# Kernel tuning notes

Measured on AMD Instinct MI355X. Metric: run time of the kernel, lower is better.

The kernel has to match this reference:

```python
import jax, jax.numpy as jnp
import numpy as np
import math

NUM_HEADS = 16
EMBED = 1024
B, S = 128, 512


def setup_inputs() -> dict:
    key = jax.random.key(0)
    ks = jax.random.split(key, 9)
    scale = 1.0 / math.sqrt(EMBED)
    return {
        "queries": jax.random.normal(ks[0], (B, S, EMBED), dtype=jnp.float32),
        "keys": jax.random.normal(ks[1], (B, S, EMBED), dtype=jnp.float32),
        "values": jax.random.normal(ks[2], (B, S, EMBED), dtype=jnp.float32),
        "Wq": jax.random.normal(ks[3], (EMBED, EMBED), dtype=jnp.float32) * scale,
        "bq": jax.random.normal(ks[4], (EMBED,), dtype=jnp.float32) * scale,
        "Wk": jax.random.normal(ks[5], (EMBED, EMBED), dtype=jnp.float32) * scale,
        "bk": jax.random.normal(ks[6], (EMBED,), dtype=jnp.float32) * scale,
        "Wv": jax.random.normal(ks[7], (EMBED, EMBED), dtype=jnp.float32) * scale,
        "bv": jax.random.normal(ks[8], (EMBED,), dtype=jnp.float32) * scale,
    }


def reference(queries, keys, values, Wq, bq, Wk, bk, Wv, bv):
    H = NUM_HEADS
    E = queries.shape[-1]
    d = E // H
    # torch nn.Linear: y = x @ W.T + b
    q = queries @ Wq.T + bq  # [B, S, E]
    k = keys @ Wk.T + bk
    v = values @ Wv.T + bv
    n_q = q.shape[1]
    n_k = k.shape[1]
    n_v = v.shape[1]
    # Faithful to the original: reshape with seq-len as the LEADING dim,
    # which reinterprets the (B, S, E) buffer as (S, B, H, d).
    q = q.reshape(n_q, -1, H, d)  # [S, B, H, d]
    k = k.reshape(n_k, -1, H, d)
    # attention over the second (batch-like) axis; scores: [S, H, B, B]
    scores = jnp.einsum('nqhd,nkhd->nhqk', q, k) / math.sqrt(d)
    attn = jax.nn.softmax(scores, axis=-1)
    v = v.reshape(n_v, -1, H, d)  # [S, B, H, d]
    out = jnp.einsum('nhql,nlhd->nqhd', attn, v)  # [S, B, H, d]
    n_a = out.shape[0]
    return out.reshape(-1, n_a, H * d)  # [B, S, E]
```

## Files before the change

### kernel.cpp

```cpp
#include <hip/hip_runtime.h>
#include <hip/hip_bf16.h>

typedef unsigned short u16;
typedef __attribute__((ext_vector_type(8))) short bf16x8;
typedef __attribute__((ext_vector_type(4))) float f32x4;
typedef __attribute__((ext_vector_type(4))) float vfloat4;
typedef __attribute__((ext_vector_type(4))) unsigned short ushort4v;
typedef __attribute__((ext_vector_type(8))) unsigned short ushort8v;

#define DEV __device__ __forceinline__
#define AS1 __attribute__((address_space(1)))
#define AS3 __attribute__((address_space(3)))

#define BARRIER()  __builtin_amdgcn_s_barrier()
#define LGKM0()    asm volatile("s_waitcnt lgkmcnt(0)" ::: "memory")
#define VMCNT2()   asm volatile("s_waitcnt vmcnt(2)" ::: "memory")
#define SCHED0()   __builtin_amdgcn_sched_barrier(0)

DEV u16 f2bf(float f) {
    union { float f; unsigned u; } v; v.f = f;
    unsigned r = v.u + 0x7FFFu + ((v.u >> 16) & 1u);
    return (u16)(r >> 16);
}

DEV void gload_lds16(const void* g, void* l) {
    __builtin_amdgcn_global_load_lds((const AS1 unsigned int*)g,
                                     (AS3 unsigned int*)l, 16, 0, 0);
}

static constexpr int KDIM = 1024;
static constexpr int NROW = 65536;

__global__ __launch_bounds__(256)
void cvt_f32_bf16(const float* __restrict__ src, u16* __restrict__ dst, unsigned n8)
{
    unsigned stride = gridDim.x * blockDim.x;
    for (unsigned i = blockIdx.x * blockDim.x + threadIdx.x; i < n8; i += stride) {
        size_t base = (size_t)i * 8;
        vfloat4 a = *(const vfloat4*)(src + base);
        vfloat4 b = *(const vfloat4*)(src + base + 4);
        ushort8v o;
#pragma unroll
        for (int j = 0; j < 4; ++j) { o[j] = f2bf(a[j]); o[j + 4] = f2bf(b[j]); }
        *(ushort8v*)(dst + base) = o;
    }
}

__global__ __launch_bounds__(512)
__attribute__((amdgpu_waves_per_eu(1, 2)))
void proj_gemm_8ph(const u16* __restrict__ X, const u16* __restrict__ W,
                   const float* __restrict__ bias, u16* __restrict__ Y)
{
    __shared__ __align__(16) u16 As[2][256 * 64];
    __shared__ __align__(16) u16 Bs[2][256 * 64];

    int bx = blockIdx.x;
    int wg = (bx & 7) * 128 + (bx >> 3);
    int bm = wg >> 2;
    int bn = wg & 3;

    int tid  = threadIdx.x;
    int lane = tid & 63;
    int wid  = tid >> 6;
    int wm   = wid >> 2;
    int wn   = wid & 3;
    int l15  = lane & 15;
    int l4   = lane >> 4;

    const u16* Xp = X + (size_t)bm * 256 * KDIM;
    const u16* Wp = W + (size_t)bn * 256 * KDIM;

    int srow_in = tid >> 3;
    int scol16  = (tid & 7) ^ (srow_in & 7);

    f32x4 acc[8][4] = {};

#define STAGE(lds, gbase, slot, h, kt)                                           \
    {                                                                            \
        const u16* src_ = (gbase) + (size_t)((h) * 128 + srow_in) * KDIM         \
                          + (kt) * 64 + scol16 * 8;                              \
        gload_lds16(src_, &lds[slot][((h) * 128 + wid * 8) * 64]);               \
        gload_lds16(src_ + (size_t)64 * KDIM,                                    \
                    &lds[slot][((h) * 128 + 64 + wid * 8) * 64]);                \
    }

#define READ_AF(slot, mh)                                                        \
    {                                                                            \
        _Pragma("unroll")                                                        \
        for (int mi = 0; mi < 4; ++mi) {                                         \
            int row = wm * 128 + (mh) * 64 + mi * 16 + l15;                      \
            unsigned o0 = (unsigned)(row * 128 + l4 * 16) ^ (unsigned)((row & 7) << 4); \
            af[mi][0] = *(const bf16x8*)((const char*)As[slot] + o0);            \
            af[mi][1] = *(const bf16x8*)((const char*)As[slot] + (o0 ^ 64u));    \
        }                                                                        \
    }

#define READ_BF(dst, slot, nh)                                                   \
    {                                                                            \
        _Pragma("unroll")                                                        \
        for (int ni = 0; ni < 2; ++ni) {                                         \
            int row = wn * 64 + (nh) * 32 + ni * 16 + l15;                       \
            unsigned o0 = (unsigned)(row * 128 + l4 * 16) ^ (unsigned)((row & 7) << 4); \
            dst[ni][0] = *(const bf16x8*)((const char*)Bs[slot] + o0);           \
            dst[ni][1] = *(const bf16x8*)((const char*)Bs[slot] + (o0 ^ 64u));   \
        }                                                                        \
    }

#define MFMA_Q(mlo, bb, nlo)                                                     \
    __builtin_amdgcn_s_setprio(1);                                               \
    _Pragma("unroll")                                                            \
    for (int mi = 0; mi < 4; ++mi) {                                             \
        _Pragma("unroll")                                                        \
        for (int ni = 0; ni < 2; ++ni) {                                         \
            _Pragma("unroll")                                                    \
            for (int kk = 0; kk < 2; ++kk)                                       \
                acc[(mlo) + mi][(nlo) + ni] = __builtin_amdgcn_mfma_f32_16x16x32_bf16( \
                    af[mi][kk], bb[ni][kk], acc[(mlo) + mi][(nlo) + ni], 0, 0, 0); \
        }                                                                        \
    }                                                                            \
    __builtin_amdgcn_s_setprio(0);

    STAGE(As, Xp, 0, 0, 0);
    STAGE(As, Xp, 0, 1, 0);
    STAGE(Bs, Wp, 0, 0, 0);
    STAGE(Bs, Wp, 0, 1, 0);
    STAGE(As, Xp, 1, 0, 1);
    VMCNT2();
    BARRIER();

    for (int it = 0; it < 8; ++it) {
        int kt1 = 2 * it + 1;
        int kt2 = (2 * it + 2 < 16) ? 2 * it + 2 : 15;
        int kt3 = (2 * it + 3 < 16) ? 2 * it + 3 : 15;
        bf16x8 af[4][2], b0[2][2], b1[2][2];

        READ_AF(0, 0); READ_BF(b0, 0, 0);
        STAGE(As, Xp, 1, 1, kt1);
        BARRIER(); LGKM0(); SCHED0();
        MFMA_Q(0, b0, 0);
        BARRIER();

        READ_BF(b1, 0, 1);
        STAGE(Bs, Wp, 1, 0, kt1);
        BARRIER(); LGKM0(); SCHED0();
        MFMA_Q(0, b1, 2);
        BARRIER();

        READ_AF(0, 1);
        STAGE(Bs, Wp, 1, 1, kt1);
        BARRIER(); LGKM0(); SCHED0();
        MFMA_Q(4, b1, 2);
        BARRIER();

        STAGE(As, Xp, 0, 0, kt2);
        MFMA_Q(4, b0, 0);
        VMCNT2();
        BARRIER();

        READ_AF(1, 0); READ_BF(b0, 1, 0);
        STAGE(As, Xp, 0, 1, kt2);
        BARRIER(); LGKM0(); SCHED0();
        MFMA_Q(0, b0, 0);
        BARRIER();

        READ_BF(b1, 1, 1);
        STAGE(Bs, Wp, 0, 0, kt2);
        BARRIER(); LGKM0(); SCHED0();
        MFMA_Q(0, b1, 2);
        BARRIER();

        READ_AF(1, 1);
        STAGE(Bs, Wp, 0, 1, kt2);
        BARRIER(); LGKM0(); SCHED0();
        MFMA_Q(4, b1, 2);
        BARRIER();

        STAGE(As, Xp, 1, 0, kt3);
        MFMA_Q(4, b0, 0);
        VMCNT2();
        BARRIER();
    }

#pragma unroll
    for (int ni = 0; ni < 4; ++ni) {
        int col = bn * 256 + wn * 64 + ni * 16 + l15;
        float bv = bias[col];
#pragma unroll
        for (int mi = 0; mi < 8; ++mi) {
            int row0 = bm * 256 + wm * 128 + mi * 16 + l4 * 4;
#pragma unroll
            for (int r = 0; r < 4; ++r)
                Y[(size_t)(row0 + r) * KDIM + col] = f2bf(acc[mi][ni][r] + bv);
        }
    }
#undef STAGE
#undef READ_AF
#undef READ_BF
#undef MFMA_Q
}

__global__ __launch_bounds__(256)
void proj_gemm(const float* __restrict__ X, const float* __restrict__ W,
               const float* __restrict__ bias, u16* __restrict__ Y)
{
    __shared__ u16 As[128 * 64];
    __shared__ u16 Bs[128 * 64];

    int bx = blockIdx.x;
    int wg = (bx & 7) * 512 + (bx >> 3);
    int bm = wg >> 3;
    int bn = wg & 7;

    int tid  = threadIdx.x;
    int lane = tid & 63;
    int wid  = tid >> 6;
    int wrow = (wid >> 1) * 64;
    int wcol = (wid & 1) * 64;
    int l15 = lane & 15;
    int l4  = lane >> 4;

    int srow = tid >> 4;
    int scol = (tid & 15) * 4;

    const float* Xp = X + (size_t)bm * 128 * KDIM;
    const float* Wp = W + (size_t)bn * 128 * KDIM;

    f32x4 acc[4][4] = {};

    for (int k0 = 0; k0 < KDIM; k0 += 64) {
        __syncthreads();
#pragma unroll
        for (int r = 0; r < 8; ++r) {
            int row = r * 16 + srow;
            vfloat4 a = *(const vfloat4*)(Xp + (size_t)row * KDIM + k0 + scol);
            vfloat4 b = *(const vfloat4*)(Wp + (size_t)row * KDIM + k0 + scol);
            ushort4v ap, bp;
#pragma unroll
            for (int j = 0; j < 4; ++j) { ap[j] = f2bf(a[j]); bp[j] = f2bf(b[j]); }
            unsigned off = (unsigned)(row * 128 + scol * 2) ^ (unsigned)((row & 7) << 4);
            *(ushort4v*)((char*)As + off) = ap;
            *(ushort4v*)((char*)Bs + off) = bp;
        }
        __syncthreads();
#pragma unroll
        for (int kk = 0; kk < 2; ++kk) {
            bf16x8 af[4], bfr[4];
#pragma unroll
            for (int mi = 0; mi < 4; ++mi) {
                int row = wrow + mi * 16 + l15;
                unsigned off = (unsigned)(row * 128 + kk * 64 + l4 * 16) ^ (unsigned)((row & 7) << 4);
                af[mi] = *(const bf16x8*)((char*)As + off);
            }
#pragma unroll
            for (int ni = 0; ni < 4; ++ni) {
                int row = wcol + ni * 16 + l15;
                unsigned off = (unsigned)(row * 128 + kk * 64 + l4 * 16) ^ (unsigned)((row & 7) << 4);
                bfr[ni] = *(const bf16x8*)((char*)Bs + off);
            }
#pragma unroll
            for (int mi = 0; mi < 4; ++mi)
#pragma unroll
                for (int ni = 0; ni < 4; ++ni)
                    acc[mi][ni] = __builtin_amdgcn_mfma_f32_16x16x32_bf16(
                        af[mi], bfr[ni], acc[mi][ni], 0, 0, 0);
        }
    }

#pragma unroll
    for (int ni = 0; ni < 4; ++ni) {
        int col = bn * 128 + wcol + ni * 16 + l15;
        float bv = bias[col];
#pragma unroll
        for (int mi = 0; mi < 4; ++mi) {
            int row0 = bm * 128 + wrow + mi * 16 + l4 * 4;
#pragma unroll
            for (int r = 0; r < 4; ++r)
                Y[(size_t)(row0 + r) * KDIM + col] = f2bf(acc[mi][ni][r] + bv);
        }
    }
}

__global__ __launch_bounds__(256)
void attn_kernel(const u16* __restrict__ Qg, const u16* __restrict__ Kg,
                 const u16* __restrict__ Vg, float* __restrict__ Out)
{
    __shared__ u16 Qs[128 * 64];
    __shared__ u16 KVs[64 * 136];
    __shared__ u16 Ps[128 * 136];

    int g = blockIdx.x >> 4;
    int h = blockIdx.x & 15;

    int tid  = threadIdx.x;
    int lane = tid & 63;
    int wid  = tid >> 6;
    int l15 = lane & 15, l4 = lane >> 4;
    int qbase = wid * 32;

    size_t rowbase = (size_t)g * 128 * 1024 + (size_t)h * 64;

    {
        int r  = tid >> 1;
        int c0 = (tid & 1) * 32;
        const u16* qsrc = Qg + rowbase + (size_t)r * 1024 + c0;
        const u16* ksrc = Kg + rowbase + (size_t)r * 1024 + c0;
#pragma unroll
        for (int i = 0; i < 4; ++i) {
            ushort8v qv = *(const ushort8v*)(qsrc + i * 8);
            ushort8v kv = *(const ushort8v*)(ksrc + i * 8);
            unsigned off = (unsigned)(r * 128 + (c0 + i * 8) * 2) ^ (unsigned)((r & 7) << 4);
            *(ushort8v*)((char*)Qs + off) = qv;
            *(ushort8v*)((char*)KVs + off) = kv;
        }
    }
    __syncthreads();

    f32x4 st[8][2] = {};
#pragma unroll
    for (int kk = 0; kk < 2; ++kk) {
        bf16x8 kf[8];
#pragma unroll
        for (int mi = 0; mi < 8; ++mi) {
            int row = mi * 16 + l15;
            unsigned off = (unsigned)(row * 128 + kk * 64 + l4 * 16) ^ (unsigned)((row & 7) << 4);
            kf[mi] = *(const bf16x8*)((char*)KVs + off);
        }
#pragma unroll
        for (int qi = 0; qi < 2; ++qi) {
            int row = qbase + qi * 16 + l15;
            unsigned off = (unsigned)(row * 128 + kk * 64 + l4 * 16) ^ (unsigned)((row & 7) << 4);
            bf16x8 qf = *(const bf16x8*)((char*)Qs + off);
#pragma unroll
            for (int mi = 0; mi < 8; ++mi)
                st[mi][qi] = __builtin_amdgcn_mfma_f32_16x16x32_bf16(kf[mi], qf, st[mi][qi], 0, 0, 0);
        }
    }
    __syncthreads();

    {
        int r  = tid >> 1;
        int c0 = (tid & 1) * 32;
        const u16* vsrc = Vg + rowbase + (size_t)r * 1024 + c0;
#pragma unroll
        for (int i = 0; i < 4; ++i) {
            ushort8v vv = *(const ushort8v*)(vsrc + i * 8);
#pragma unroll
            for (int e = 0; e < 8; ++e)
                KVs[(c0 + i * 8 + e) * 136 + r] = vv[e];
        }
    }

    const float cexp = 0.125f * 1.44269504088896f;
#pragma unroll
    for (int qi = 0; qi < 2; ++qi) {
        float m = -3.0e38f;
#pragma unroll
        for (int mi = 0; mi < 8; ++mi)
#pragma unroll
            for (int r = 0; r < 4; ++r) m = fmaxf(m, st[mi][qi][r]);
        m = fmaxf(m, __shfl_xor(m, 16));
        m = fmaxf(m, __shfl_xor(m, 32));
        float s = 0.f;
#pragma unroll
        for (int mi = 0; mi < 8; ++mi)
#pragma unroll
            for (int r = 0; r < 4; ++r) {
                float p = exp2f((st[mi][qi][r] - m) * cexp);
                st[mi][qi][r] = p;
                s += p;
            }
        s += __shfl_xor(s, 16);
        s += __shfl_xor(s, 32);
        float inv = 1.0f / s;
        int q = qbase + qi * 16 + l15;
#pragma unroll
        for (int mi = 0; mi < 8; ++mi) {
            ushort4v pp;
#pragma unroll
            for (int r = 0; r < 4; ++r) pp[r] = f2bf(st[mi][qi][r] * inv);
            *(ushort4v*)((char*)Ps + (unsigned)(q * 272 + mi * 32 + l4 * 8)) = pp;
        }
    }
    __syncthreads();

    f32x4 o[2][4] = {};
#pragma unroll
    for (int kk = 0; kk < 4; ++kk) {
        bf16x8 pa[2];
#pragma unroll
        for (int mf = 0; mf < 2; ++mf) {
            int q = qbase + mf * 16 + l15;
            pa[mf] = *(const bf16x8*)((char*)Ps + (unsigned)(q * 272 + kk * 64 + l4 * 16));
        }
#pragma unroll
        for (int nf = 0; nf < 4; ++nf) {
            int d = nf * 16 + l15;
            bf16x8 vb = *(const bf16x8*)((char*)KVs + (unsigned)(d * 272 + kk * 64 + l4 * 16));
#pragma unroll
            for (int mf = 0; mf < 2; ++mf)
                o[mf][nf] = __builtin_amdgcn_mfma_f32_16x16x32_bf16(pa[mf], vb, o[mf][nf], 0, 0, 0);
        }
    }

#pragma unroll
    for (int mf = 0; mf < 2; ++mf)
#pragma unroll
        for (int nf = 0; nf < 4; ++nf) {
            int d  = nf * 16 + l15;
            int q0 = qbase + mf * 16 + l4 * 4;
#pragma unroll
            for (int r = 0; r < 4; ++r)
                Out[(size_t)(g * 128 + q0 + r) * 1024 + h * 64 + d] = o[mf][nf][r];
        }
}

extern "C" void kernel_launch(void* const* d_in, const int* in_sizes, int n_in,
                              void* d_out, int out_size, void* d_ws, size_t ws_size,
                              hipStream_t stream)
{
    const float* Xq = (const float*)d_in[0];
    const float* Xk = (const float*)d_in[1];
    const float* Xv = (const float*)d_in[2];
    const float* Wq = (const float*)d_in[3];
    const float* bq = (const float*)d_in[4];
    const float* Wk = (const float*)d_in[5];
    const float* bk = (const float*)d_in[6];
    const float* Wv = (const float*)d_in[7];
    const float* bv = (const float*)d_in[8];

    const size_t NE = (size_t)NROW * KDIM;
    const size_t WE = (size_t)KDIM * KDIM;

    u16* Qw = (u16*)d_ws;
    u16* Kw = Qw + NE;
    u16* Vw = Kw + NE;

    size_t need = NE * 2 * 3 + NE * 2 + WE * 2 * 3;

    if (ws_size >= need) {
        u16* Xb  = Vw + NE;
        u16* Wb0 = Xb + NE;
        u16* Wb1 = Wb0 + WE;
        u16* Wb2 = Wb1 + WE;

        cvt_f32_bf16<<<dim3(512),  dim3(256), 0, stream>>>(Wq, Wb0, (unsigned)(WE / 8));
        cvt_f32_bf16<<<dim3(512),  dim3(256), 0, stream>>>(Wk, Wb1, (unsigned)(WE / 8));
        cvt_f32_bf16<<<dim3(512),  dim3(256), 0, stream>>>(Wv, Wb2, (unsigned)(WE / 8));

        cvt_f32_bf16<<<dim3(2048), dim3(256), 0, stream>>>(Xq, Xb, (unsigned)(NE / 8));
        proj_gemm_8ph<<<dim3(1024), dim3(512), 0, stream>>>(Xb, Wb0, bq, Qw);
        cvt_f32_bf16<<<dim3(2048), dim3(256), 0, stream>>>(Xk, Xb, (unsigned)(NE / 8));
        proj_gemm_8ph<<<dim3(1024), dim3(512), 0, stream>>>(Xb, Wb1, bk, Kw);
        cvt_f32_bf16<<<dim3(2048), dim3(256), 0, stream>>>(Xv, Xb, (unsigned)(NE / 8));
        proj_gemm_8ph<<<dim3(1024), dim3(512), 0, stream>>>(Xb, Wb2, bv, Vw);
    } else {
        proj_gemm<<<dim3(4096), dim3(256), 0, stream>>>(Xq, Wq, bq, Qw);
        proj_gemm<<<dim3(4096), dim3(256), 0, stream>>>(Xk, Wk, bk, Kw);
        proj_gemm<<<dim3(4096), dim3(256), 0, stream>>>(Xv, Wv, bv, Vw);
    }

    attn_kernel<<<dim3(512 * 16), dim3(256), 0, stream>>>(Qw, Kw, Vw, (float*)d_out);
}
```

Baseline: 926.8 us.

## Restructure GEMM prefetch schedule to preload two full K-tiles and reorder stage loads

The projection GEMM prologue now stages both K-tiles fully before the main loop, and the loop reorders which A/B half-tiles are loaded at each sub-step so that B tiles for the next-next step are issued earlier. The vmcnt wait moves to vmcnt(4) before the last MFMA quarter, and a final vmcnt(0) drains outstanding loads. The goal is deeper prefetch so global loads are hidden behind MFMA work, at the risk of LDS write-after-read hazards if buffer reuse timing is wrong.

```diff
diff --git a/kernel.cpp b/kernel.cpp
--- a/kernel.cpp
+++ b/kernel.cpp
@@ -14,7 +14,8 @@
 
 #define BARRIER()  __builtin_amdgcn_s_barrier()
 #define LGKM0()    asm volatile("s_waitcnt lgkmcnt(0)" ::: "memory")
-#define VMCNT2()   asm volatile("s_waitcnt vmcnt(2)" ::: "memory")
+#define VMCNT0()   asm volatile("s_waitcnt vmcnt(0)" ::: "memory")
+#define VMCNT4()   asm volatile("s_waitcnt vmcnt(4)" ::: "memory")
 #define SCHED0()   __builtin_amdgcn_sched_barrier(0)
 
 DEV u16 f2bf(float f) {
@@ -125,61 +126,65 @@
     STAGE(Bs, Wp, 0, 0, 0);
     STAGE(Bs, Wp, 0, 1, 0);
     STAGE(As, Xp, 1, 0, 1);
-    VMCNT2();
+    STAGE(As, Xp, 1, 1, 1);
+    STAGE(Bs, Wp, 1, 0, 1);
+    STAGE(Bs, Wp, 1, 1, 1);
+    VMCNT0();
     BARRIER();
 
     for (int it = 0; it < 8; ++it) {
-        int kt1 = 2 * it + 1;
-        int kt2 = (2 * it + 2 < 16) ? 2 * it + 2 : 15;
-        int kt3 = (2 * it + 3 < 16) ? 2 * it + 3 : 15;
+        int c12 = 2 * it + 1;
+        int c36 = (2 * it + 2 < 16) ? 2 * it + 2 : 15;
+        int c78 = (2 * it + 3 < 16) ? 2 * it + 3 : 15;
         bf16x8 af[4][2], b0[2][2], b1[2][2];
 
         READ_AF(0, 0); READ_BF(b0, 0, 0);
-        STAGE(As, Xp, 1, 1, kt1);
+        STAGE(As, Xp, 1, 0, c12);
         BARRIER(); LGKM0(); SCHED0();
         MFMA_Q(0, b0, 0);
         BARRIER();
 
         READ_BF(b1, 0, 1);
-        STAGE(Bs, Wp, 1, 0, kt1);
+        STAGE(As, Xp, 1, 1, c12);
         BARRIER(); LGKM0(); SCHED0();
         MFMA_Q(0, b1, 2);
         BARRIER();
 
         READ_AF(0, 1);
-        STAGE(Bs, Wp, 1, 1, kt1);
+        STAGE(Bs, Wp, 0, 0, c36);
         BARRIER(); LGKM0(); SCHED0();
         MFMA_Q(4, b1, 2);
         BARRIER();
 
-        STAGE(As, Xp, 0, 0, kt2);
+        STAGE(Bs, Wp, 0, 1, c36);
+        VMCNT4(); BARRIER(); SCHED0();
         MFMA_Q(4, b0, 0);
-        VMCNT2();
         BARRIER();
 
         READ_AF(1, 0); READ_BF(b0, 1, 0);
-        STAGE(As, Xp, 0, 1, kt2);
+        STAGE(As, Xp, 0, 0, c36);
         BARRIER(); LGKM0(); SCHED0();
         MFMA_Q(0, b0, 0);
         BARRIER();
 
         READ_BF(b1, 1, 1);
-        STAGE(Bs, Wp, 0, 0, kt2);
+        STAGE(As, Xp, 0, 1, c36);
         BARRIER(); LGKM0(); SCHED0();
         MFMA_Q(0, b1, 2);
         BARRIER();
 
         READ_AF(1, 1);
-        STAGE(Bs, Wp, 0, 1, kt2);
+        STAGE(Bs, Wp, 1, 0, c78);
         BARRIER(); LGKM0(); SCHED0();
         MFMA_Q(4, b1, 2);
         BARRIER();
 
-        STAGE(As, Xp, 1, 0, kt3);
+        STAGE(Bs, Wp, 1, 1, c78);
+        VMCNT4(); BARRIER(); SCHED0();
         MFMA_Q(4, b0, 0);
-        VMCNT2();
-        BARRIER();
-    }
+        BARRIER();
+    }
+    VMCNT0();
 
 #pragma unroll
     for (int ni = 0; ni < 4; ++ni) {
```

Measured after the change: 937.9 us. Within noise of the previous version (+1.2%).
